# Kernel optimization log

Hardware: AMD Instinct MI355X
Metric: run time of the kernel (lower is better)

The kernel has to match this reference:

```python
import jax, jax.numpy as jnp
import numpy as np

NUM_HEADS = 8
NEG_SLOPE = 0.2


def typed_linear(x, W, etype):
    # x: [E, din], W: [T, din, dout], etype: [E] int. Grouped (per-edge-type) linear,
    # computed as T dense GEMMs with a per-edge select (T is small and static).
    out = jnp.zeros((x.shape[0], W.shape[2]), x.dtype)
    for t in range(W.shape[0]):
        out = out + jnp.where((etype == t)[:, None], x @ W[t], jnp.zeros((), x.dtype))
    return out


def setup_inputs() -> dict:
    key = jax.random.key(0)
    ks = jax.random.split(key, 9)
    N, E, IN = 50000, 800000, 128
    H, D = NUM_HEADS, 16
    HD = H * D  # 128
    T = 8  # num edge types
    s = 0.05
    return {
        "x": jax.random.normal(ks[0], (N, IN), jnp.float32),
        "src": jax.random.randint(ks[1], (E,), 0, N),
        "dst": jax.random.randint(ks[2], (E,), 0, N),
        "etype": jax.random.randint(ks[3], (E,), 0, T),
        "W_w": jax.random.normal(ks[4], (T, IN, HD), jnp.float32) * s,
        "W_al": jax.random.normal(ks[5], (T, HD, HD), jnp.float32) * s,
        "W_ar": jax.random.normal(ks[6], (T, HD, HD), jnp.float32) * s,
        "W_res": jax.random.normal(ks[7], (IN, HD), jnp.float32) * s,
        "b_res": jnp.zeros((HD,), jnp.float32),
    }


def reference(x, src, dst, etype, W_w, W_al, W_ar, W_res, b_res):
    N = x.shape[0]
    HD = W_w.shape[2]
    H = NUM_HEADS
    D = HD // H

    m = x[src]                                   # copy_u gather: [E, in]
    feat = typed_linear(m, W_w, etype)           # [E, H*D]
    h = feat                                     # dropout p=0 (eval/deterministic)

    # per-head attention logits
    h_l = typed_linear(h, W_al, etype).reshape(-1, H, D).sum(-1)  # [E, H]
    h_r = typed_linear(h, W_ar, etype).reshape(-1, H, D).sum(-1)  # [E, H]
    att = jax.nn.leaky_relu(h_l + h_r, NEG_SLOPE)

    # edge_softmax: segment softmax over incoming edges of each dst node
    att_max = jax.ops.segment_max(att, dst, num_segments=N)       # [N, H]
    att_exp = jnp.exp(att - att_max[dst])
    denom = jax.ops.segment_sum(att_exp, dst, num_segments=N)
    att = att_exp / denom[dst]                                    # [E, H]

    # NOTE: in the original source, 'alpha' is computed and stored in edata but the
    # aggregation copies edata 'm' (== h), so alpha never reaches the output.
    alpha = jnp.einsum('ehd,eh->ed', h.reshape(-1, H, D), att)    # [E, D] (dead)
    del alpha

    # update_all(copy_e('m'), sum): scatter-sum of h into dst nodes
    emb = jax.ops.segment_sum(h, dst, num_segments=N)             # [N, H*D]

    out = emb + x @ W_res + b_res                                 # residual
    return jax.nn.elu(out)
```

## Files before the change

kernel.cpp:

```cpp
#include <hip/hip_runtime.h>
#include <hip/hip_bf16.h>


#define KW 1152
#define CAP 3072
#define CHUNK 2048

typedef __bf16 bf16x8 __attribute__((ext_vector_type(8)));
typedef float f32x4 __attribute__((ext_vector_type(4)));
typedef float f32x2 __attribute__((ext_vector_type(2)));

__device__ __forceinline__ void gload_lds16(const void* g, void* l) {
  __builtin_amdgcn_global_load_lds(
      (const __attribute__((address_space(1))) unsigned int*)g,
      (__attribute__((address_space(3))) unsigned int*)l, 16, 0, 0);
}

__global__ __launch_bounds__(512) void k_binA(
    const int* __restrict__ src, const int* __restrict__ dst,
    const int* __restrict__ et, int* __restrict__ gCount,
    int* __restrict__ bucketBuf, int E) {
  __shared__ int buf[CHUNK];
  __shared__ short bkt[CHUNK];
  __shared__ int hist[512], sc[512], ls[512], cur[512], gb[512];
  const int tid = threadIdx.x;
  const int base = blockIdx.x * CHUNK;
  const int cnt = min(CHUNK, E - base);

  hist[tid] = 0;
  __syncthreads();
  for (int j = tid; j < cnt; j += 512) atomicAdd(&hist[dst[base + j] >> 7], 1);
  __syncthreads();
  sc[tid] = hist[tid];
  __syncthreads();
  for (int off = 1; off < 512; off <<= 1) {
    int t = (tid >= off) ? sc[tid - off] : 0;
    __syncthreads();
    if (tid >= off) sc[tid] += t;
    __syncthreads();
  }
  ls[tid] = sc[tid] - hist[tid];
  cur[tid] = ls[tid];
  gb[tid] = (hist[tid] > 0) ? atomicAdd(&gCount[tid], hist[tid]) : 0;
  __syncthreads();
  for (int j = tid; j < cnt; j += 512) {
    int e = base + j;
    int d = dst[e];
    int b = d >> 7;
    int pos = atomicAdd(&cur[b], 1);
    buf[pos] = (src[e] << 10) | (et[e] << 7) | (d & 127);
    bkt[pos] = (short)b;
  }
  __syncthreads();
  for (int j = tid; j < cnt; j += 512) {
    int b = bkt[j];
    bucketBuf[b * CAP + gb[b] + (j - ls[b])] = buf[j];
  }
}

__global__ __launch_bounds__(512) void k_scanC(
    const int* __restrict__ gCount, int* __restrict__ coarseBase,
    int* __restrict__ rowstart, int N, int E) {
  __shared__ int sc[512], h[512];
  int tid = threadIdx.x;
  h[tid] = gCount[tid];
  sc[tid] = h[tid];
  __syncthreads();
  for (int off = 1; off < 512; off <<= 1) {
    int t = (tid >= off) ? sc[tid - off] : 0;
    __syncthreads();
    if (tid >= off) sc[tid] += t;
    __syncthreads();
  }
  coarseBase[tid] = sc[tid] - h[tid];
  if (tid == 0) rowstart[N] = E;
}

__global__ __launch_bounds__(512) void k_sortB(
    const int* __restrict__ bucketBuf, const int* __restrict__ gCount,
    const int* __restrict__ coarseBase, int* __restrict__ rowstart,
    int* __restrict__ packed, int N) {
  __shared__ int raw[CAP];
  __shared__ int srt[CAP];
  __shared__ int hist[128], sc[128], bs[128], cur[128];
  const int b = blockIdx.x;
  const int tid = threadIdx.x;
  const int cnt = min(gCount[b], CAP);
  const int base = coarseBase[b];

  if (tid < 128) hist[tid] = 0;
  __syncthreads();
  for (int j = tid; j < cnt; j += 512) {
    int p = bucketBuf[b * CAP + j];
    raw[j] = p;
    atomicAdd(&hist[p & 127], 1);
  }
  __syncthreads();
  if (tid < 128) sc[tid] = hist[tid];
  __syncthreads();
  for (int off = 1; off < 128; off <<= 1) {
    int t = (tid < 128 && tid >= off) ? sc[tid - off] : 0;
    __syncthreads();
    if (tid < 128 && tid >= off) sc[tid] += t;
    __syncthreads();
  }
  if (tid < 128) {
    bs[tid] = sc[tid] - hist[tid];
    cur[tid] = bs[tid];
    int node = b * 128 + tid;
    if (node < N) rowstart[node] = base + bs[tid];
  }
  __syncthreads();
  for (int j = tid; j < cnt; j += 512) {
    int p = raw[j];
    int pos = atomicAdd(&cur[p & 127], 1);
    srt[pos] = p;
  }
  __syncthreads();
  for (int j = tid; j < cnt; j += 512) {
    int p = srt[j];
    packed[base + j] = (p >> 10) * 576 + (((p >> 7) & 7) << 6);
  }
}

__global__ void k_xcast(const float* __restrict__ x, ushort4* __restrict__ xb4,
                        int n4, int npad4) {
  int i = blockIdx.x * 256 + threadIdx.x;
  if (i >= npad4) return;
  ushort4 o = {0, 0, 0, 0};
  if (i < n4) {
    f32x4 v = *(const f32x4*)(x + i * 4);
    __hip_bfloat16 h0 = __float2bfloat16(v[0]), h1 = __float2bfloat16(v[1]);
    __hip_bfloat16 h2 = __float2bfloat16(v[2]), h3 = __float2bfloat16(v[3]);
    o.x = *(unsigned short*)&h0; o.y = *(unsigned short*)&h1;
    o.z = *(unsigned short*)&h2; o.w = *(unsigned short*)&h3;
  }
  xb4[i] = o;
}

__global__ void k_wb(const float* __restrict__ Ww, const float* __restrict__ Wres,
                     __hip_bfloat16* __restrict__ Wb) {
  int o = blockIdx.x * 256 + threadIdx.x;
  if (o >= KW * 128) return;
  int nn = o >> 7, kk = o & 127;
  float v = (nn < 1024) ? Ww[(nn >> 7) * 16384 + kk * 128 + (nn & 127)]
                        : Wres[kk * 128 + (nn & 127)];
  Wb[o] = __float2bfloat16(v);
}

__global__ __launch_bounds__(512) void k_ygemm(
    const __hip_bfloat16* __restrict__ xb, const __hip_bfloat16* __restrict__ Wb,
    unsigned short* __restrict__ y) {
  __shared__ __align__(16) unsigned short As[128 * 128];
  __shared__ __align__(16) unsigned short Bs[128 * 128];
  const int tid = threadIdx.x;
  const int lane = tid & 63;
  const int wid = tid >> 6;
  const int wr = wid >> 2, wc = wid & 3;
  const long row0 = (long)blockIdx.x * 128;
  const int nb0 = blockIdx.y * 128;

  const char* xbb = (const char*)xb;
  const char* wbb = (const char*)Wb;
  char* asb = (char*)As;
  char* bsb = (char*)Bs;

#pragma unroll
  for (int i = 0; i < 8; ++i) {
    int c = i * 512 + tid;
    int half = c >> 11;
    int cc = c & 2047;
    int r = cc >> 4, colb = (cc & 15) << 4;
    int srcb = colb ^ ((r & 7) << 4);
    if (half == 0)
      gload_lds16(xbb + (row0 + r) * 256 + srcb, asb + r * 256 + colb);
    else
      gload_lds16(wbb + (long)(nb0 + r) * 256 + srcb, bsb + r * 256 + colb);
  }
  asm volatile("s_waitcnt vmcnt(0)" ::: "memory");
  __syncthreads();

  f32x4 acc[4][2] = {};
#pragma unroll
  for (int ks = 0; ks < 4; ++ks) {
    const int cb = ks * 64 + ((lane >> 4) << 4);
    bf16x8 af[4], bfr[2];
#pragma unroll
    for (int mi = 0; mi < 4; ++mi) {
      int row = wr * 64 + mi * 16 + (lane & 15);
      af[mi] = *(const bf16x8*)(asb + ((row * 256 + cb) ^ ((row & 7) << 4)));
    }
#pragma unroll
    for (int ni = 0; ni < 2; ++ni) {
      int rowb = wc * 32 + ni * 16 + (lane & 15);
      bfr[ni] = *(const bf16x8*)(bsb + ((rowb * 256 + cb) ^ ((rowb & 7) << 4)));
    }
#pragma unroll
    for (int mi = 0; mi < 4; ++mi)
#pragma unroll
      for (int ni = 0; ni < 2; ++ni)
        acc[mi][ni] = __builtin_amdgcn_mfma_f32_16x16x32_bf16(
            af[mi], bfr[ni], acc[mi][ni], 0, 0, 0);
  }

#pragma unroll
  for (int mi = 0; mi < 4; ++mi)
#pragma unroll
    for (int ni = 0; ni < 2; ++ni) {
      int col = nb0 + wc * 32 + ni * 16 + (lane & 15);
      long rb = row0 + wr * 64 + mi * 16 + ((lane >> 4) << 2);
      f32x4 v = acc[mi][ni];
#pragma unroll
      for (int q = 0; q < 4; ++q) {
        __hip_bfloat16 h = __float2bfloat16(v[q]);
        __builtin_nontemporal_store(*(unsigned short*)&h, y + (rb + q) * KW + col);
      }
    }
}

__global__ __launch_bounds__(256) void k_scat(
    const ushort2* __restrict__ y2, const int* __restrict__ rowstart,
    const int* __restrict__ packed, const float* __restrict__ bres,
    float* __restrict__ out, int N) {
  const int w = threadIdx.x >> 6, lane = threadIdx.x & 63;
  const int n = blockIdx.x * 4 + w;
  if (n >= N) return;
  float ax = 0.f, ay = 0.f;
  int e = rowstart[n];
  const int end = rowstart[n + 1];
  for (; e + 16 <= end; e += 16) {
    int p[16];
#pragma unroll
    for (int j = 0; j < 16; ++j) p[j] = packed[e + j];
    ushort2 r[16];
#pragma unroll
    for (int j = 0; j < 16; ++j) r[j] = y2[p[j] + lane];
    __builtin_amdgcn_sched_barrier(0);
#pragma unroll
    for (int j = 0; j < 16; ++j) {
      ax += __uint_as_float((unsigned)r[j].x << 16);
      ay += __uint_as_float((unsigned)r[j].y << 16);
    }
  }
  {
    int p[4];
    ushort2 r[4];
    for (; e + 4 <= end; e += 4) {
#pragma unroll
      for (int j = 0; j < 4; ++j) p[j] = packed[e + j];
#pragma unroll
      for (int j = 0; j < 4; ++j) r[j] = y2[p[j] + lane];
      __builtin_amdgcn_sched_barrier(0);
#pragma unroll
      for (int j = 0; j < 4; ++j) {
        ax += __uint_as_float((unsigned)r[j].x << 16);
        ay += __uint_as_float((unsigned)r[j].y << 16);
      }
    }
  }
  for (; e < end; ++e) {
    ushort2 r = y2[packed[e] + lane];
    ax += __uint_as_float((unsigned)r.x << 16);
    ay += __uint_as_float((unsigned)r.y << 16);
  }
  ushort2 rr = y2[n * 576 + 512 + lane];
  ax += __uint_as_float((unsigned)rr.x << 16) + bres[2 * lane];
  ay += __uint_as_float((unsigned)rr.y << 16) + bres[2 * lane + 1];
  f32x2 o;
  o[0] = ax > 0.f ? ax : (expf(ax) - 1.f);
  o[1] = ay > 0.f ? ay : (expf(ay) - 1.f);
  __builtin_nontemporal_store(o, (f32x2*)(out + (long)n * 128 + 2 * lane));
}

extern "C" void kernel_launch(void* const* d_in, const int* in_sizes, int n_in,
                              void* d_out, int out_size, void* d_ws, size_t ws_size,
                              hipStream_t stream) {
  const float* x = (const float*)d_in[0];
  const int* src = (const int*)d_in[1];
  const int* dst = (const int*)d_in[2];
  const int* et = (const int*)d_in[3];
  const float* Ww = (const float*)d_in[4];
  const float* Wres = (const float*)d_in[7];
  const float* bres = (const float*)d_in[8];
  float* out = (float*)d_out;

  const int N = in_sizes[0] / 128;
  const int E = in_sizes[1];
  const int padM = ((N + 127) / 128) * 128;
  const int COARSE = (N + 127) >> 7;

  char* ws = (char*)d_ws;
  size_t off = 0;
  auto take = [&](size_t b) {
    char* p = ws + off;
    off = (off + b + 255) & ~(size_t)255;
    return p;
  };
  __hip_bfloat16* y = (__hip_bfloat16*)take((size_t)padM * KW * 2);
  __hip_bfloat16* Wb = (__hip_bfloat16*)take((size_t)KW * 128 * 2);
  __hip_bfloat16* xb = (__hip_bfloat16*)take((size_t)padM * 128 * 2);
  int* rowstart = (int*)take((size_t)(N + 1) * 4);
  int* gCount = (int*)take(512 * 4);
  int* coarseBase = (int*)take(512 * 4);
  int* packed = (int*)take((size_t)E * 4);
  int* bucketBuf = (int*)y;

  hipMemsetAsync(gCount, 0, 512 * 4, stream);
  k_binA<<<(E + CHUNK - 1) / CHUNK, 512, 0, stream>>>(src, dst, et, gCount, bucketBuf, E);
  k_scanC<<<1, 512, 0, stream>>>(gCount, coarseBase, rowstart, N, E);
  k_sortB<<<COARSE, 512, 0, stream>>>(bucketBuf, gCount, coarseBase, rowstart, packed, N);
  k_wb<<<(KW * 128 + 255) / 256, 256, 0, stream>>>(Ww, Wres, Wb);
  const int n4 = N * 128 / 4, npad4 = padM * 128 / 4;
  k_xcast<<<(npad4 + 255) / 256, 256, 0, stream>>>(x, (ushort4*)xb, n4, npad4);
  dim3 gy(padM / 128, 9);
  k_ygemm<<<gy, 512, 0, stream>>>(xb, Wb, (unsigned short*)y);
  k_scat<<<(N + 3) / 4, 256, 0, stream>>>((const ushort2*)y, rowstart, packed, bres, out, N);
}
```

Measured before the change: 220.5 us.

## Loop GEMM over all column groups per block and widen scatter gathers to 8 bytes

```diff
diff --git a/kernel.cpp b/kernel.cpp
--- a/kernel.cpp
+++ b/kernel.cpp
@@ -8,13 +8,15 @@
 
 typedef __bf16 bf16x8 __attribute__((ext_vector_type(8)));
 typedef float f32x4 __attribute__((ext_vector_type(4)));
-typedef float f32x2 __attribute__((ext_vector_type(2)));
 
 __device__ __forceinline__ void gload_lds16(const void* g, void* l) {
   __builtin_amdgcn_global_load_lds(
       (const __attribute__((address_space(1))) unsigned int*)g,
       (__attribute__((address_space(3))) unsigned int*)l, 16, 0, 0);
 }
+
+__device__ __forceinline__ float uflo(unsigned u) { return __uint_as_float(u << 16); }
+__device__ __forceinline__ float ufhi(unsigned u) { return __uint_as_float(u & 0xffff0000u); }
 
 __global__ __launch_bounds__(512) void k_binA(
     const int* __restrict__ src, const int* __restrict__ dst,
@@ -119,7 +121,7 @@
   __syncthreads();
   for (int j = tid; j < cnt; j += 512) {
     int p = srt[j];
-    packed[base + j] = (p >> 10) * 576 + (((p >> 7) & 7) << 6);
+    packed[base + j] = (p >> 10) * 288 + (((p >> 7) & 7) << 5);
   }
 }
 
@@ -158,7 +160,6 @@
   const int wid = tid >> 6;
   const int wr = wid >> 2, wc = wid & 3;
   const long row0 = (long)blockIdx.x * 128;
-  const int nb0 = blockIdx.y * 128;
 
   const char* xbb = (const char*)xb;
   const char* wbb = (const char*)Wb;
@@ -166,110 +167,117 @@
   char* bsb = (char*)Bs;
 
 #pragma unroll
-  for (int i = 0; i < 8; ++i) {
+  for (int i = 0; i < 4; ++i) {
     int c = i * 512 + tid;
-    int half = c >> 11;
-    int cc = c & 2047;
-    int r = cc >> 4, colb = (cc & 15) << 4;
+    int r = c >> 4, colb = (c & 15) << 4;
     int srcb = colb ^ ((r & 7) << 4);
-    if (half == 0)
-      gload_lds16(xbb + (row0 + r) * 256 + srcb, asb + r * 256 + colb);
-    else
-      gload_lds16(wbb + (long)(nb0 + r) * 256 + srcb, bsb + r * 256 + colb);
-  }
-  asm volatile("s_waitcnt vmcnt(0)" ::: "memory");
-  __syncthreads();
-
-  f32x4 acc[4][2] = {};
-#pragma unroll
-  for (int ks = 0; ks < 4; ++ks) {
-    const int cb = ks * 64 + ((lane >> 4) << 4);
-    bf16x8 af[4], bfr[2];
-#pragma unroll
-    for (int mi = 0; mi < 4; ++mi) {
-      int row = wr * 64 + mi * 16 + (lane & 15);
-      af[mi] = *(const bf16x8*)(asb + ((row * 256 + cb) ^ ((row & 7) << 4)));
-    }
-#pragma unroll
-    for (int ni = 0; ni < 2; ++ni) {
-      int rowb = wc * 32 + ni * 16 + (lane & 15);
-      bfr[ni] = *(const bf16x8*)(bsb + ((rowb * 256 + cb) ^ ((rowb & 7) << 4)));
-    }
+    gload_lds16(xbb + (row0 + r) * 256 + srcb, asb + r * 256 + colb);
+  }
+
+  for (int g = 0; g < 9; ++g) {
+#pragma unroll
+    for (int i = 0; i < 4; ++i) {
+      int c = i * 512 + tid;
+      int r = c >> 4, colb = (c & 15) << 4;
+      int srcb = colb ^ ((r & 7) << 4);
+      gload_lds16(wbb + (long)(g * 128 + r) * 256 + srcb, bsb + r * 256 + colb);
+    }
+    asm volatile("s_waitcnt vmcnt(0)" ::: "memory");
+    __syncthreads();
+
+    f32x4 acc[4][2] = {};
+#pragma unroll
+    for (int ks = 0; ks < 4; ++ks) {
+      const int cb = ks * 64 + ((lane >> 4) << 4);
+      bf16x8 af[4], bfr[2];
+#pragma unroll
+      for (int mi = 0; mi < 4; ++mi) {
+        int row = wr * 64 + mi * 16 + (lane & 15);
+        af[mi] = *(const bf16x8*)(asb + ((row * 256 + cb) ^ ((row & 7) << 4)));
+      }
+#pragma unroll
+      for (int ni = 0; ni < 2; ++ni) {
+        int rowb = wc * 32 + ni * 16 + (lane & 15);
+        bfr[ni] = *(const bf16x8*)(bsb + ((rowb * 256 + cb) ^ ((rowb & 7) << 4)));
+      }
+#pragma unroll
+      for (int mi = 0; mi < 4; ++mi)
+#pragma unroll
+        for (int ni = 0; ni < 2; ++ni)
+          acc[mi][ni] = __builtin_amdgcn_mfma_f32_16x16x32_bf16(
+              af[mi], bfr[ni], acc[mi][ni], 0, 0, 0);
+    }
+
 #pragma unroll
     for (int mi = 0; mi < 4; ++mi)
 #pragma unroll
-      for (int ni = 0; ni < 2; ++ni)
-        acc[mi][ni] = __builtin_amdgcn_mfma_f32_16x16x32_bf16(
-            af[mi], bfr[ni], acc[mi][ni], 0, 0, 0);
-  }
-
-#pragma unroll
-  for (int mi = 0; mi < 4; ++mi)
-#pragma unroll
-    for (int ni = 0; ni < 2; ++ni) {
-      int col = nb0 + wc * 32 + ni * 16 + (lane & 15);
-      long rb = row0 + wr * 64 + mi * 16 + ((lane >> 4) << 2);
-      f32x4 v = acc[mi][ni];
-#pragma unroll
-      for (int q = 0; q < 4; ++q) {
-        __hip_bfloat16 h = __float2bfloat16(v[q]);
-        __builtin_nontemporal_store(*(unsigned short*)&h, y + (rb + q) * KW + col);
+      for (int ni = 0; ni < 2; ++ni) {
+        int col = g * 128 + wc * 32 + ni * 16 + (lane & 15);
+        long rb = row0 + wr * 64 + mi * 16 + ((lane >> 4) << 2);
+        f32x4 v = acc[mi][ni];
+#pragma unroll
+        for (int q = 0; q < 4; ++q) {
+          __hip_bfloat16 h = __float2bfloat16(v[q]);
+          y[(rb + q) * KW + col] = *(unsigned short*)&h;
+        }
       }
-    }
+    __syncthreads();
+  }
 }
 
 __global__ __launch_bounds__(256) void k_scat(
-    const ushort2* __restrict__ y2, const int* __restrict__ rowstart,
+    const uint2* __restrict__ y4, const int* __restrict__ rowstart,
     const int* __restrict__ packed, const float* __restrict__ bres,
     float* __restrict__ out, int N) {
   const int w = threadIdx.x >> 6, lane = threadIdx.x & 63;
   const int n = blockIdx.x * 4 + w;
   if (n >= N) return;
-  float ax = 0.f, ay = 0.f;
+  const int half = lane >> 5;
+  const int sub = lane & 31;
+  f32x4 a = {0.f, 0.f, 0.f, 0.f};
   int e = rowstart[n];
   const int end = rowstart[n + 1];
+
   for (; e + 16 <= end; e += 16) {
-    int p[16];
-#pragma unroll
-    for (int j = 0; j < 16; ++j) p[j] = packed[e + j];
-    ushort2 r[16];
-#pragma unroll
-    for (int j = 0; j < 16; ++j) r[j] = y2[p[j] + lane];
+    uint2 r[8];
+#pragma unroll
+    for (int k = 0; k < 8; ++k) {
+      int p = packed[e + 2 * k + half];
+      r[k] = y4[p + sub];
+    }
     __builtin_amdgcn_sched_barrier(0);
 #pragma unroll
-    for (int j = 0; j < 16; ++j) {
-      ax += __uint_as_float((unsigned)r[j].x << 16);
-      ay += __uint_as_float((unsigned)r[j].y << 16);
-    }
-  }
-  {
-    int p[4];
-    ushort2 r[4];
-    for (; e + 4 <= end; e += 4) {
-#pragma unroll
-      for (int j = 0; j < 4; ++j) p[j] = packed[e + j];
-#pragma unroll
-      for (int j = 0; j < 4; ++j) r[j] = y2[p[j] + lane];
-      __builtin_amdgcn_sched_barrier(0);
-#pragma unroll
-      for (int j = 0; j < 4; ++j) {
-        ax += __uint_as_float((unsigned)r[j].x << 16);
-        ay += __uint_as_float((unsigned)r[j].y << 16);
-      }
-    }
-  }
-  for (; e < end; ++e) {
-    ushort2 r = y2[packed[e] + lane];
-    ax += __uint_as_float((unsigned)r.x << 16);
-    ay += __uint_as_float((unsigned)r.y << 16);
-  }
-  ushort2 rr = y2[n * 576 + 512 + lane];
-  ax += __uint_as_float((unsigned)rr.x << 16) + bres[2 * lane];
-  ay += __uint_as_float((unsigned)rr.y << 16) + bres[2 * lane + 1];
-  f32x2 o;
-  o[0] = ax > 0.f ? ax : (expf(ax) - 1.f);
-  o[1] = ay > 0.f ? ay : (expf(ay) - 1.f);
-  __builtin_nontemporal_store(o, (f32x2*)(out + (long)n * 128 + 2 * lane));
+    for (int k = 0; k < 8; ++k) {
+      a[0] += uflo(r[k].x); a[1] += ufhi(r[k].x);
+      a[2] += uflo(r[k].y); a[3] += ufhi(r[k].y);
+    }
+  }
+  for (; e + 2 <= end; e += 2) {
+    int p = packed[e + half];
+    uint2 r = y4[p + sub];
+    a[0] += uflo(r.x); a[1] += ufhi(r.x);
+    a[2] += uflo(r.y); a[3] += ufhi(r.y);
+  }
+  if (e < end) {
+    int p = packed[e];
+    uint2 r = y4[p + sub];
+    if (!half) {
+      a[0] += uflo(r.x); a[1] += ufhi(r.x);
+      a[2] += uflo(r.y); a[3] += ufhi(r.y);
+    }
+  }
+#pragma unroll
+  for (int i = 0; i < 4; ++i) a[i] += __shfl_xor(a[i], 32);
+
+  uint2 rr = y4[n * 288 + 256 + sub];
+  f32x4 b4 = *(const f32x4*)(bres + sub * 4);
+  a[0] += uflo(rr.x) + b4[0]; a[1] += ufhi(rr.x) + b4[1];
+  a[2] += uflo(rr.y) + b4[2]; a[3] += ufhi(rr.y) + b4[3];
+  f32x4 o;
+#pragma unroll
+  for (int i = 0; i < 4; ++i) o[i] = a[i] > 0.f ? a[i] : (expf(a[i]) - 1.f);
+  if (!half)
+    __builtin_nontemporal_store(o, (f32x4*)(out + (long)n * 128 + sub * 4));
 }
 
 extern "C" void kernel_launch(void* const* d_in, const int* in_sizes, int n_in,
@@ -312,7 +320,6 @@
   k_wb<<<(KW * 128 + 255) / 256, 256, 0, stream>>>(Ww, Wres, Wb);
   const int n4 = N * 128 / 4, npad4 = padM * 128 / 4;
   k_xcast<<<(npad4 + 255) / 256, 256, 0, stream>>>(x, (ushort4*)xb, n4, npad4);
-  dim3 gy(padM / 128, 9);
-  k_ygemm<<<gy, 512, 0, stream>>>(xb, Wb, (unsigned short*)y);
-  k_scat<<<(N + 3) / 4, 256, 0, stream>>>((const ushort2*)y, rowstart, packed, bres, out, N);
-}
+  k_ygemm<<<padM / 128, 512, 0, stream>>>(xb, Wb, (unsigned short*)y);
+  k_scat<<<(N + 3) / 4, 256, 0, stream>>>((const uint2*)y, rowstart, packed, bres, out, N);
+}
```

After: 198.4 us. -10.0%, faster.
